# Kernel optimization log

Hardware: AMD Instinct MI355X
Metric: run time of the kernel (lower is better)

Reference implementation:

```python
import jax, jax.numpy as jnp
import numpy as np

NEG_SLOPE = 0.2  # PyG GATConv default


def _gat_conv(x, src, dst, W, a_src, a_dst, bias, concat):
    # x: [N, F_in]; W: [H*C, F_in]; a_src/a_dst: [H, C]; src/dst: [E]
    n = x.shape[0]
    H, C = a_src.shape
    h = (x @ W.T).reshape(n, H, C)                       # [N, H, C]
    al_src = (h * a_src[None]).sum(-1)                   # [N, H]
    al_dst = (h * a_dst[None]).sum(-1)                   # [N, H]
    e = jax.nn.leaky_relu(al_src[src] + al_dst[dst], NEG_SLOPE)  # [E, H]
    # scatter-softmax over incoming edges of each dst node
    m = jax.ops.segment_max(e, dst, num_segments=n)      # [N, H]
    e = jnp.exp(e - m[dst])
    denom = jax.ops.segment_sum(e, dst, num_segments=n)  # [N, H]
    alpha = e / denom[dst]                               # [E, H]
    out = jax.ops.segment_sum(alpha[:, :, None] * h[src], dst, num_segments=n)  # [N, H, C]
    if concat:
        out = out.reshape(n, H * C)
    else:
        out = out.mean(axis=1)
    return out + bias


def setup_inputs() -> dict:
    key = jax.random.key(0)
    ks = jax.random.split(key, 16)
    N, E = 20000, 640000
    IN, HID, HEADS, OUT, HLSTM, NCLS = 256, 32, 4, 64, 32, 1
    s = 0.1
    return {
        "x": jax.random.normal(ks[0], (N, IN), jnp.float32),
        "conv1_w": jax.random.normal(ks[1], (HID * HEADS, IN), jnp.float32) * s,
        "conv1_att_src": jax.random.normal(ks[2], (HEADS, HID), jnp.float32) * s,
        "conv1_att_dst": jax.random.normal(ks[3], (HEADS, HID), jnp.float32) * s,
        "conv1_bias": jnp.zeros((HID * HEADS,), jnp.float32),
        "conv2_w": jax.random.normal(ks[4], (OUT, HID * HEADS), jnp.float32) * s,
        "conv2_att_src": jax.random.normal(ks[5], (1, OUT), jnp.float32) * s,
        "conv2_att_dst": jax.random.normal(ks[6], (1, OUT), jnp.float32) * s,
        "conv2_bias": jnp.zeros((OUT,), jnp.float32),
        "lstm_w_ih": jax.random.normal(ks[7], (4 * HLSTM, OUT), jnp.float32) * s,
        "lstm_w_hh": jax.random.normal(ks[8], (4 * HLSTM, HLSTM), jnp.float32) * s,
        "lstm_b_ih": jnp.zeros((4 * HLSTM,), jnp.float32),
        "lstm_b_hh": jnp.zeros((4 * HLSTM,), jnp.float32),
        "fc_w": jax.random.normal(ks[9], (NCLS, HLSTM), jnp.float32) * s,
        "fc_b": jnp.zeros((NCLS,), jnp.float32),
        "edge_index": jax.random.randint(ks[10], (2, E), 0, N, jnp.int64),
    }


def reference(x, conv1_w, conv1_att_src, conv1_att_dst, conv1_bias,
              conv2_w, conv2_att_src, conv2_att_dst, conv2_bias,
              lstm_w_ih, lstm_w_hh, lstm_b_ih, lstm_b_hh,
              fc_w, fc_b, edge_index):
    N = x.shape[0]
    loops = jnp.arange(N, dtype=edge_index.dtype)  # add_self_loops=True (PyG default)
    src = jnp.concatenate([edge_index[0], loops])
    dst = jnp.concatenate([edge_index[1], loops])

    h = _gat_conv(x, src, dst, conv1_w, conv1_att_src, conv1_att_dst, conv1_bias, concat=True)
    h = jax.nn.elu(h)
    h = _gat_conv(h, src, dst, conv2_w, conv2_att_src, conv2_att_dst, conv2_bias, concat=False)

    # LSTM over the node sequence, batch=1 (x.view(-1, N, out_dim))
    Hs = lstm_w_hh.shape[1]
    pre = h @ lstm_w_ih.T + (lstm_b_ih + lstm_b_hh)      # [N, 4H] input projections

    def step(carry, p):
        hp, cp = carry
        g = p + hp @ lstm_w_hh.T
        i, f, gg, o = jnp.split(g, 4)
        c = jax.nn.sigmoid(f) * cp + jax.nn.sigmoid(i) * jnp.tanh(gg)
        hn = jax.nn.sigmoid(o) * jnp.tanh(c)
        return (hn, c), hn

    init = (jnp.zeros((Hs,), x.dtype), jnp.zeros((Hs,), x.dtype))
    _, seq = jax.lax.scan(step, init, pre)               # [N, H]
    out = seq @ fc_w.T + fc_b                            # [N, num_classes]
    return out[None]                                     # [1, N, num_classes]
```

## Files before the change

### kernel.cpp

```cpp
#include <hip/hip_runtime.h>
#include <hip/hip_bf16.h>
#include <hip/hip_fp16.h>
#include <cstdint>
#include <cstddef>

#define LOG2E 1.44269504088896340736f
#define SLOTW 128
#define SCAP 32

typedef float v2f __attribute__((ext_vector_type(2)));
typedef _Float16 f16x8 __attribute__((ext_vector_type(8)));
typedef float f32x4 __attribute__((ext_vector_type(4)));

__global__ __launch_bounds__(256, 2)
void gemm1_mfma(const float* __restrict__ A, const float* __restrict__ B,
                const float* __restrict__ asrc, const float* __restrict__ adst,
                float* __restrict__ als, float* __restrict__ ald,
                __half* __restrict__ Ch, int N,
                const int* __restrict__ esrc, const int* __restrict__ edst,
                int* __restrict__ cnt, unsigned short* __restrict__ slots,
                int E, int gemmBlocks) {
  if ((int)blockIdx.x >= gemmBlocks) {
    int base = ((int)blockIdx.x - gemmBlocks) * 1024 + (int)threadIdx.x * 4;
    if (base + 3 < E) {
      int4 ss = *(const int4*)(esrc + base);
      int4 dd = *(const int4*)(edst + base);
      int p0 = atomicAdd(&cnt[dd.x], 1);
      int p1 = atomicAdd(&cnt[N + dd.y], 1);
      int p2 = atomicAdd(&cnt[2 * N + dd.z], 1);
      int p3 = atomicAdd(&cnt[3 * N + dd.w], 1);
      if (p0 < SCAP) slots[(size_t)dd.x * SLOTW + p0] = (unsigned short)ss.x;
      if (p1 < SCAP) slots[(size_t)dd.y * SLOTW + 32 + p1] = (unsigned short)ss.y;
      if (p2 < SCAP) slots[(size_t)dd.z * SLOTW + 64 + p2] = (unsigned short)ss.z;
      if (p3 < SCAP) slots[(size_t)dd.w * SLOTW + 96 + p3] = (unsigned short)ss.w;
    } else if (base < E) {
      for (int t = base; t < E; ++t) {
        int s = esrc[t], d = edst[t];
        int j = t & 3;
        int pos = atomicAdd(&cnt[j * N + d], 1);
        if (pos < SCAP) slots[(size_t)d * SLOTW + j * 32 + pos] = (unsigned short)s;
      }
    }
    return;
  }
  constexpr int M = 128, K = 256, TN = 32, KB = 64;
  constexpr int LDH = 72;
  constexpr int RF = 2, CF = 2;
  constexpr int NS = K / KB;

  __shared__ __align__(16) _Float16 As[TN * LDH];
  __shared__ __align__(16) _Float16 Bs[M * LDH];

  const int tid = threadIdx.x;
  const int n0 = blockIdx.x * TN;
  const int w = tid >> 6, lane = tid & 63;
  const int lr = lane & 15, lg = lane >> 4;
  const int colbase = w * 32;

  const int ar = tid >> 3;
  const int ak = (tid & 7) * 8;
  const int gnA = n0 + ar;

  f32x4 acc[RF][CF];
#pragma unroll
  for (int rf = 0; rf < RF; ++rf)
#pragma unroll
    for (int cf = 0; cf < CF; ++cf) acc[rf][cf] = (f32x4){0.f, 0.f, 0.f, 0.f};

  float4 pa0, pa1;
  float4 pb[8];

  const float* aRow = A + (size_t)gnA * K + ak;

#define LOADG(k0)                                                              \
  do {                                                                         \
    if (gnA < N) { pa0 = *(const float4*)(aRow + (k0));                        \
                   pa1 = *(const float4*)(aRow + (k0) + 4); }                  \
    else { pa0 = make_float4(0.f,0.f,0.f,0.f); pa1 = pa0; }                    \
    _Pragma("unroll")                                                          \
    for (int c = 0; c < 4; ++c) {                                              \
      int cid = c * 256 + tid;                                                 \
      int brow = cid >> 3, bk = (cid & 7) * 8;                                 \
      const float* bp = B + (size_t)brow * K + (k0) + bk;                      \
      pb[2*c]   = *(const float4*)bp;                                          \
      pb[2*c+1] = *(const float4*)(bp + 4);                                    \
    }                                                                          \
  } while (0)

  LOADG(0);
  for (int s = 0; s < NS; ++s) {
    {
      f16x8 h;
      h[0]=(_Float16)pa0.x; h[1]=(_Float16)pa0.y; h[2]=(_Float16)pa0.z; h[3]=(_Float16)pa0.w;
      h[4]=(_Float16)pa1.x; h[5]=(_Float16)pa1.y; h[6]=(_Float16)pa1.z; h[7]=(_Float16)pa1.w;
      *(f16x8*)&As[ar * LDH + ak] = h;
#pragma unroll
      for (int c = 0; c < 4; ++c) {
        int cid = c * 256 + tid;
        int brow = cid >> 3, bk = (cid & 7) * 8;
        f16x8 hb;
        hb[0]=(_Float16)pb[2*c].x; hb[1]=(_Float16)pb[2*c].y;
        hb[2]=(_Float16)pb[2*c].z; hb[3]=(_Float16)pb[2*c].w;
        hb[4]=(_Float16)pb[2*c+1].x; hb[5]=(_Float16)pb[2*c+1].y;
        hb[6]=(_Float16)pb[2*c+1].z; hb[7]=(_Float16)pb[2*c+1].w;
        *(f16x8*)&Bs[brow * LDH + bk] = hb;
      }
    }
    __syncthreads();
    if (s + 1 < NS) LOADG((s + 1) * KB);
    {
      f16x8 af[2][RF], bf[2][CF];
#pragma unroll
      for (int ks = 0; ks < 2; ++ks) {
#pragma unroll
        for (int rf = 0; rf < RF; ++rf)
          af[ks][rf] = *(const f16x8*)&As[(rf * 16 + lr) * LDH + ks * 32 + 8 * lg];
#pragma unroll
        for (int cf = 0; cf < CF; ++cf)
          bf[ks][cf] = *(const f16x8*)&Bs[(colbase + cf * 16 + lr) * LDH + ks * 32 + 8 * lg];
      }
#pragma unroll
      for (int ks = 0; ks < 2; ++ks)
#pragma unroll
        for (int rf = 0; rf < RF; ++rf)
#pragma unroll
          for (int cf = 0; cf < CF; ++cf)
            acc[rf][cf] = __builtin_amdgcn_mfma_f32_16x16x32_f16(af[ks][rf], bf[ks][cf], acc[rf][cf], 0, 0, 0);
    }
    __syncthreads();
  }
#undef LOADG

#pragma unroll
  for (int rf = 0; rf < RF; ++rf) {
#pragma unroll
    for (int reg = 0; reg < 4; ++reg) {
      const int gr = n0 + rf * 16 + lg * 4 + reg;
      if (gr < N) {
#pragma unroll
        for (int cf = 0; cf < CF; ++cf)
          Ch[(size_t)gr * M + colbase + cf * 16 + lr] = __float2half(acc[rf][cf][reg]);
      }
    }
  }
  {
    float as_v[CF], ad_v[CF];
#pragma unroll
    for (int cf = 0; cf < CF; ++cf) {
      as_v[cf] = asrc[colbase + cf * 16 + lr];
      ad_v[cf] = adst[colbase + cf * 16 + lr];
    }
#pragma unroll
    for (int rf = 0; rf < RF; ++rf) {
#pragma unroll
      for (int reg = 0; reg < 4; ++reg) {
        const int gr = n0 + rf * 16 + lg * 4 + reg;
        float ps = acc[rf][0][reg] * as_v[0] + acc[rf][1][reg] * as_v[1];
        float pd = acc[rf][0][reg] * ad_v[0] + acc[rf][1][reg] * ad_v[1];
#pragma unroll
        for (int m = 1; m < 16; m <<= 1) { ps += __shfl_xor(ps, m); pd += __shfl_xor(pd, m); }
        if (lr == 0 && gr < N) {
          als[(size_t)gr * 4 + w] = ps;
          ald[(size_t)gr * 4 + w] = pd;
        }
      }
    }
  }
}

template<int M, int K, bool BIAS, bool AL, int H, bool HOUT, bool SCAT>
__global__ __launch_bounds__(256)
void gemm_mfma(const float* __restrict__ A, const float* __restrict__ B,
               const float* __restrict__ bias0, const float* __restrict__ bias1,
               const float* __restrict__ asrc, const float* __restrict__ adst,
               float* __restrict__ als, float* __restrict__ ald,
               float* __restrict__ C, __half* __restrict__ Ch, int N,
               const int* __restrict__ esrc, const int* __restrict__ edst,
               int* __restrict__ cnt, unsigned short* __restrict__ slots,
               int E, int gemmBlocks) {
  constexpr int TN = 64, KB = 32;
  constexpr int LDH = 40;
  constexpr int WCOL = (M >= 128) ? 2 : 1;
  constexpr int WROW = 4 / WCOL;
  constexpr int RT = TN / WROW;
  constexpr int CTW = M / WCOL;
  constexpr int RF = RT / 16;
  constexpr int CF = CTW / 16;

  __shared__ __align__(16) _Float16 As[TN * LDH];
  __shared__ __align__(16) _Float16 Bs[M * LDH];

  const int tid = threadIdx.x;
  const int n0 = blockIdx.x * TN;
  const int w = tid >> 6, lane = tid & 63;
  const int wr = w / WCOL, wc = w % WCOL;
  const int lr = lane & 15, lg = lane >> 4;

  f32x4 acc[RF][CF];
#pragma unroll
  for (int rf = 0; rf < RF; ++rf)
#pragma unroll
    for (int cf = 0; cf < CF; ++cf) acc[rf][cf] = (f32x4){0.f, 0.f, 0.f, 0.f};

  const int arow = tid >> 2, akq = (tid & 3) * 8;
  const int bcol = tid >> 1, bkq = (tid & 1) * 16;

  for (int k0 = 0; k0 < K; k0 += KB) {
    {
      int gn = n0 + arow;
      float4 v0 = make_float4(0.f, 0.f, 0.f, 0.f), v1 = v0;
      if (gn < N) {
        const float* ap = A + (size_t)gn * K + k0 + akq;
        v0 = *(const float4*)ap;
        v1 = *(const float4*)(ap + 4);
      }
      f16x8 h;
      h[0] = (_Float16)v0.x; h[1] = (_Float16)v0.y; h[2] = (_Float16)v0.z; h[3] = (_Float16)v0.w;
      h[4] = (_Float16)v1.x; h[5] = (_Float16)v1.y; h[6] = (_Float16)v1.z; h[7] = (_Float16)v1.w;
      *(f16x8*)&As[arow * LDH + akq] = h;
    }
    if (bcol < M) {
      const float* bp = B + (size_t)bcol * K + k0 + bkq;
      float4 v0 = *(const float4*)bp;
      float4 v1 = *(const float4*)(bp + 4);
      float4 v2 = *(const float4*)(bp + 8);
      float4 v3 = *(const float4*)(bp + 12);
      f16x8 h0, h1;
      h0[0] = (_Float16)v0.x; h0[1] = (_Float16)v0.y; h0[2] = (_Float16)v0.z; h0[3] = (_Float16)v0.w;
      h0[4] = (_Float16)v1.x; h0[5] = (_Float16)v1.y; h0[6] = (_Float16)v1.z; h0[7] = (_Float16)v1.w;
      h1[0] = (_Float16)v2.x; h1[1] = (_Float16)v2.y; h1[2] = (_Float16)v2.z; h1[3] = (_Float16)v2.w;
      h1[4] = (_Float16)v3.x; h1[5] = (_Float16)v3.y; h1[6] = (_Float16)v3.z; h1[7] = (_Float16)v3.w;
      *(f16x8*)&Bs[bcol * LDH + bkq] = h0;
      *(f16x8*)&Bs[bcol * LDH + bkq + 8] = h1;
    }
    __syncthreads();
    f16x8 af[RF], bf[CF];
#pragma unroll
    for (int rf = 0; rf < RF; ++rf)
      af[rf] = *(const f16x8*)&As[(wr * RT + rf * 16 + lr) * LDH + 8 * lg];
#pragma unroll
    for (int cf = 0; cf < CF; ++cf)
      bf[cf] = *(const f16x8*)&Bs[(wc * CTW + cf * 16 + lr) * LDH + 8 * lg];
#pragma unroll
    for (int rf = 0; rf < RF; ++rf)
#pragma unroll
      for (int cf = 0; cf < CF; ++cf)
        acc[rf][cf] = __builtin_amdgcn_mfma_f32_16x16x32_f16(af[rf], bf[cf], acc[rf][cf], 0, 0, 0);
    __syncthreads();
  }

  const int colbase = wc * CTW;
  float bv[CF];
#pragma unroll
  for (int cf = 0; cf < CF; ++cf) {
    if constexpr (BIAS) bv[cf] = bias0[colbase + cf * 16 + lr] + bias1[colbase + cf * 16 + lr];
    else bv[cf] = 0.f;
  }
#pragma unroll
  for (int rf = 0; rf < RF; ++rf) {
#pragma unroll
    for (int reg = 0; reg < 4; ++reg) {
      const int gr = n0 + wr * RT + rf * 16 + lg * 4 + reg;
      if (gr < N) {
#pragma unroll
        for (int cf = 0; cf < CF; ++cf) {
          float v = acc[rf][cf][reg] + bv[cf];
          if constexpr (HOUT) Ch[(size_t)gr * M + colbase + cf * 16 + lr] = __float2half(v);
          else                C[(size_t)gr * M + colbase + cf * 16 + lr] = v;
        }
      }
    }
  }
  if constexpr (AL) {
    constexpr int CPH = M / H;
    constexpr int FPH = CPH / 16;
    constexpr int HPW = CTW / CPH;
    float as_v[CF], ad_v[CF];
#pragma unroll
    for (int cf = 0; cf < CF; ++cf) {
      as_v[cf] = asrc[colbase + cf * 16 + lr];
      ad_v[cf] = adst[colbase + cf * 16 + lr];
    }
#pragma unroll
    for (int rf = 0; rf < RF; ++rf) {
#pragma unroll
      for (int reg = 0; reg < 4; ++reg) {
        const int gr = n0 + wr * RT + rf * 16 + lg * 4 + reg;
#pragma unroll
        for (int hh = 0; hh < HPW; ++hh) {
          float ps = 0.f, pd = 0.f;
#pragma unroll
          for (int f = 0; f < FPH; ++f) {
            const int cf = hh * FPH + f;
            ps = fmaf(acc[rf][cf][reg], as_v[cf], ps);
            pd = fmaf(acc[rf][cf][reg], ad_v[cf], pd);
          }
#pragma unroll
          for (int m = 1; m < 16; m <<= 1) { ps += __shfl_xor(ps, m); pd += __shfl_xor(pd, m); }
          if (lr == 0 && gr < N) {
            const int head = (colbase + hh * CPH) / CPH;
            als[(size_t)gr * H + head] = ps;
            ald[(size_t)gr * H + head] = pd;
          }
        }
      }
    }
  }
}

template<int M, int K, bool BIAS>
__global__ __launch_bounds__(256)
void gemm_nt(const float* __restrict__ A, const float* __restrict__ B,
             const float* __restrict__ bias0, const float* __restrict__ bias1,
             float* __restrict__ C, int N) {
  constexpr int TN = 64, KB = 32;
  constexpr int CT = M / 4;
  constexpr int NR = (TN * M) / 1024;
  constexpr int WT = (M * KB) / 1024;
  __shared__ __align__(16) float xs[KB][TN + 4];
  __shared__ __align__(16) float ws[KB][M + 4];
  const int tid = threadIdx.x;
  const int tc = tid % CT, tr = tid / CT;
  const int n0 = blockIdx.x * TN;
  float acc[NR][4];
#pragma unroll
  for (int r = 0; r < NR; ++r) { acc[r][0] = acc[r][1] = acc[r][2] = acc[r][3] = 0.f; }

  for (int k0 = 0; k0 < K; k0 += KB) {
#pragma unroll
    for (int u = 0; u < 2; ++u) {
      int slot = u * 256 + tid;
      int node = slot >> 3, kv = (slot & 7) * 4;
      int gn = n0 + node;
      float4 v = make_float4(0.f, 0.f, 0.f, 0.f);
      if (gn < N) v = *(const float4*)(A + (size_t)gn * K + k0 + kv);
      xs[kv + 0][node] = v.x; xs[kv + 1][node] = v.y; xs[kv + 2][node] = v.z; xs[kv + 3][node] = v.w;
    }
#pragma unroll
    for (int u = 0; u < WT; ++u) {
      int slot = u * 256 + tid;
      int col = slot >> 3, kv = (slot & 7) * 4;
      float4 v = *(const float4*)(B + (size_t)col * K + k0 + kv);
      ws[kv + 0][col] = v.x; ws[kv + 1][col] = v.y; ws[kv + 2][col] = v.z; ws[kv + 3][col] = v.w;
    }
    __syncthreads();
#pragma unroll
    for (int kk = 0; kk < KB; ++kk) {
      float4 wv = *(const float4*)&ws[kk][tc * 4];
      float4 va = *(const float4*)&xs[kk][tr * NR];
      float4 vb = va;
      if constexpr (NR == 8) vb = *(const float4*)&xs[kk][tr * NR + 4];
      float xr[NR];
      xr[0] = va.x; xr[1] = va.y; xr[2] = va.z; xr[3] = va.w;
      if constexpr (NR == 8) { xr[4] = vb.x; xr[5] = vb.y; xr[6] = vb.z; xr[7] = vb.w; }
#pragma unroll
      for (int r = 0; r < NR; ++r) {
        acc[r][0] = fmaf(xr[r], wv.x, acc[r][0]);
        acc[r][1] = fmaf(xr[r], wv.y, acc[r][1]);
        acc[r][2] = fmaf(xr[r], wv.z, acc[r][2]);
        acc[r][3] = fmaf(xr[r], wv.w, acc[r][3]);
      }
    }
    __syncthreads();
  }
  float b[4] = {0.f, 0.f, 0.f, 0.f};
  if constexpr (BIAS) {
#pragma unroll
    for (int c = 0; c < 4; ++c) b[c] = bias0[tc * 4 + c] + bias1[tc * 4 + c];
  }
#pragma unroll
  for (int r = 0; r < NR; ++r) {
    int gn = n0 + tr * NR + r;
    if (gn < N) {
      float4 o = make_float4(acc[r][0] + b[0], acc[r][1] + b[1], acc[r][2] + b[2], acc[r][3] + b[3]);
      *(float4*)(C + (size_t)gn * M + tc * 4) = o;
    }
  }
}

template<int D, int H, bool ELU, int CAP>
__global__ __launch_bounds__(D)
void conv_edge(const __half* __restrict__ hsrc, const float* __restrict__ als,
               const float* __restrict__ ald, const float* __restrict__ bias,
               const int* __restrict__ cnt, const unsigned short* __restrict__ slots,
               const int* __restrict__ esrc, const int* __restrict__ edst, int E,
               float* __restrict__ out, int N) {
  constexpr int C = D / H;
  const int n = blockIdx.x;
  const int tid = threadIdx.x;
  const int myh = tid / C;
  const int c0 = cnt[n], c1 = cnt[N + n], c2 = cnt[2 * N + n], c3 = cnt[3 * N + n];
  const int deg_r = c0 + c1 + c2 + c3;
  const int deg = deg_r + 1;
  const bool ok = (c0 <= SCAP) && (c1 <= SCAP) && (c2 <= SCAP) && (c3 <= SCAP) && (deg <= CAP);

  __shared__ __align__(16) float lw[CAP][H];
  __shared__ int sidx[CAP];
  __shared__ float red[2][H];

  float ad[H];
#pragma unroll
  for (int hh = 0; hh < H; ++hh) ad[hh] = ald[(size_t)n * H + hh];

  float acc = 0.f;
  float myinv;
  if (ok) {
    const int b0 = c0, b1 = c0 + c1, b2 = b1 + c2;
    float sm[H];
#pragma unroll
    for (int hh = 0; hh < H; ++hh) sm[hh] = 0.f;
    const unsigned short* srow = slots + (size_t)n * SLOTW;
    for (int e = tid; e < deg; e += D) {
      int s;
      if (e == 0) s = n;
      else {
        int idx = e - 1, off;
        if (idx < b0)      off = idx;
        else if (idx < b1) off = 32 + (idx - b0);
        else if (idx < b2) off = 64 + (idx - b1);
        else               off = 96 + (idx - b2);
        s = (int)srow[off];
      }
      sidx[e] = s * (D * 2);
      if constexpr (H == 4) {
        float4 a4 = *(const float4*)(als + (size_t)s * 4);
        float l0 = a4.x + ad[0]; l0 = l0 > 0.f ? l0 : 0.2f * l0;
        float l1 = a4.y + ad[1]; l1 = l1 > 0.f ? l1 : 0.2f * l1;
        float l2 = a4.z + ad[2]; l2 = l2 > 0.f ? l2 : 0.2f * l2;
        float l3 = a4.w + ad[3]; l3 = l3 > 0.f ? l3 : 0.2f * l3;
        float w0 = __builtin_amdgcn_exp2f(LOG2E * l0);
        float w1 = __builtin_amdgcn_exp2f(LOG2E * l1);
        float w2 = __builtin_amdgcn_exp2f(LOG2E * l2);
        float w3 = __builtin_amdgcn_exp2f(LOG2E * l3);
        *(float4*)&lw[e][0] = make_float4(w0, w1, w2, w3);
        sm[0] += w0; sm[1] += w1; sm[2] += w2; sm[3] += w3;
      } else {
        float x = als[s] + ad[0];
        x = x > 0.f ? x : 0.2f * x;
        float w = __builtin_amdgcn_exp2f(LOG2E * x);
        lw[e][0] = w;
        sm[0] += w;
      }
    }
#pragma unroll
    for (int hh = 0; hh < H; ++hh) {
#pragma unroll
      for (int m = 32; m >= 1; m >>= 1) sm[hh] += __shfl_xor(sm[hh], m);
    }
    if constexpr (D > 64) {
      if ((tid & 63) == 0) {
#pragma unroll
        for (int hh = 0; hh < H; ++hh) red[tid >> 6][hh] = sm[hh];
      }
      __syncthreads();
#pragma unroll
      for (int hh = 0; hh < H; ++hh) sm[hh] = red[0][hh] + red[1][hh];
    }
    myinv = 1.0f / sm[myh];
    __syncthreads();
    const char* hb = (const char*)hsrc + (size_t)tid * 2;
#pragma unroll 8
    for (int e = 0; e < deg; ++e) {
      float w = lw[e][myh];
      int ofs = sidx[e];
      float hv = __half2float(*(const __half*)(hb + ofs));
      acc = fmaf(w, hv, acc);
    }
  } else {
    float mx[H];
#pragma unroll
    for (int hh = 0; hh < H; ++hh) {
      float xs_ = als[(size_t)n * H + hh] + ad[hh];
      xs_ = xs_ > 0.f ? xs_ : 0.2f * xs_;
      mx[hh] = xs_;
    }
    for (int e = tid; e < E; e += D) {
      if (edst[e] != n) continue;
      int s = esrc[e];
#pragma unroll
      for (int hh = 0; hh < H; ++hh) {
        float x = als[(size_t)s * H + hh] + ad[hh];
        x = x > 0.f ? x : 0.2f * x;
        mx[hh] = fmaxf(mx[hh], x);
      }
    }
#pragma unroll
    for (int hh = 0; hh < H; ++hh) {
#pragma unroll
      for (int m = 32; m >= 1; m >>= 1) mx[hh] = fmaxf(mx[hh], __shfl_xor(mx[hh], m));
    }
    if constexpr (D > 64) {
      if ((tid & 63) == 0) {
#pragma unroll
        for (int hh = 0; hh < H; ++hh) red[tid >> 6][hh] = mx[hh];
      }
      __syncthreads();
#pragma unroll
      for (int hh = 0; hh < H; ++hh) mx[hh] = fmaxf(red[0][hh], red[1][hh]);
      __syncthreads();
    }
    float sm[H];
#pragma unroll
    for (int hh = 0; hh < H; ++hh) sm[hh] = 0.f;
    if (tid == 0) {
#pragma unroll
      for (int hh = 0; hh < H; ++hh) {
        float x = als[(size_t)n * H + hh] + ad[hh];
        x = x > 0.f ? x : 0.2f * x;
        sm[hh] += __builtin_amdgcn_exp2f(LOG2E * (x - mx[hh]));
      }
    }
    for (int e = tid; e < E; e += D) {
      if (edst[e] != n) continue;
      int s = esrc[e];
#pragma unroll
      for (int hh = 0; hh < H; ++hh) {
        float x = als[(size_t)s * H + hh] + ad[hh];
        x = x > 0.f ? x : 0.2f * x;
        sm[hh] += __builtin_amdgcn_exp2f(LOG2E * (x - mx[hh]));
      }
    }
#pragma unroll
    for (int hh = 0; hh < H; ++hh) {
#pragma unroll
      for (int m = 32; m >= 1; m >>= 1) sm[hh] += __shfl_xor(sm[hh], m);
    }
    if constexpr (D > 64) {
      if ((tid & 63) == 0) {
#pragma unroll
        for (int hh = 0; hh < H; ++hh) red[tid >> 6][hh] = sm[hh];
      }
      __syncthreads();
#pragma unroll
      for (int hh = 0; hh < H; ++hh) sm[hh] = red[0][hh] + red[1][hh];
    }
    const float myad = ad[myh], mym = mx[myh];
    myinv = 1.0f / sm[myh];
    {
      float x = als[(size_t)n * H + myh] + myad;
      x = x > 0.f ? x : 0.2f * x;
      float w = __builtin_amdgcn_exp2f(LOG2E * (x - mym));
      acc = fmaf(w, __half2float(hsrc[(size_t)n * D + tid]), acc);
    }
    for (int e = 0; e < E; ++e) {
      if (edst[e] != n) continue;
      int s = esrc[e];
      float x = als[(size_t)s * H + myh] + myad;
      x = x > 0.f ? x : 0.2f * x;
      float w = __builtin_amdgcn_exp2f(LOG2E * (x - mym));
      acc = fmaf(w, __half2float(hsrc[(size_t)s * D + tid]), acc);
    }
  }
  float v = fmaf(acc, myinv, bias[tid]);
  if constexpr (ELU) v = v > 0.f ? v : (__builtin_amdgcn_exp2f(LOG2E * v) - 1.0f);
  out[(size_t)n * D + tid] = v;
}

#define LSTM_S 24
#define LSTM_W 64
__global__ __attribute__((amdgpu_waves_per_eu(1, 1))) __launch_bounds__(64)
void lstm_kernel(const float* __restrict__ pre, const float* __restrict__ whh,
                 const float* __restrict__ fcw, const float* __restrict__ fcb,
                 float* __restrict__ out, int N) {
  constexpr int U = 8;
  const int lane = threadIdx.x;
  const int k = lane & 31, half = lane >> 5;
  const int row0 = k + 32 * half;
  const int row1 = 64 + k + 32 * half;

  const int t0 = blockIdx.x * LSTM_S;
  const int tb = max(0, t0 - LSTM_W);
  const int te = min(t0 + LSTM_S, N);

  v2f wp[32];
#pragma unroll
  for (int j = 0; j < 32; ++j) {
    wp[j].x = whh[row0 * 32 + j];
    wp[j].y = whh[row1 * 32 + j];
  }
  const float mult_y = half ? -LOG2E : 2.0f * LOG2E;
  const float m1 = half ? 1.0f : -2.0f;
  const float a1c = half ? 0.0f : 1.0f;
  const float myfw = fcw[k];
  const float fcb0 = fcb[0];

  float hn = 0.f, cp = 0.f;
  float c0[U], c1[U], n0[U], n1[U];
  const float* pb = pre + (size_t)tb * 128;
#pragma unroll
  for (int u = 0; u < U; ++u) {
    c0[u] = pb[(size_t)u * 128 + row0];
    c1[u] = pb[(size_t)u * 128 + row1];
  }
#pragma unroll
  for (int u = 0; u < U; ++u) {
    n0[u] = pb[(size_t)(U + u) * 128 + row0];
    n1[u] = pb[(size_t)(U + u) * 128 + row1];
  }

#pragma unroll 1
  for (int t = tb; t < te; t += U) {
#pragma unroll
    for (int u = 0; u < U; ++u) {
      v2f acc0 = {c0[u], c1[u]};
      v2f acc1 = {0.f, 0.f}, acc2 = {0.f, 0.f}, acc3 = {0.f, 0.f};
      const int hni = __float_as_int(hn);
#pragma unroll
      for (int j = 0; j < 8; ++j) {
        float s = __int_as_float(__builtin_amdgcn_readlane(hni, 32 + j));
        v2f ss = {s, s};
        acc0 = __builtin_elementwise_fma(ss, wp[j], acc0);
      }
#pragma unroll
      for (int j = 8; j < 16; ++j) {
        float s = __int_as_float(__builtin_amdgcn_readlane(hni, 32 + j));
        v2f ss = {s, s};
        acc1 = __builtin_elementwise_fma(ss, wp[j], acc1);
      }
#pragma unroll
      for (int j = 16; j < 24; ++j) {
        float s = __int_as_float(__builtin_amdgcn_readlane(hni, 32 + j));
        v2f ss = {s, s};
        acc2 = __builtin_elementwise_fma(ss, wp[j], acc2);
      }
#pragma unroll
      for (int j = 24; j < 32; ++j) {
        float s = __int_as_float(__builtin_amdgcn_readlane(hni, 32 + j));
        v2f ss = {s, s};
        acc3 = __builtin_elementwise_fma(ss, wp[j], acc3);
      }
      v2f a01 = (acc0 + acc1) + (acc2 + acc3);
      float ax = a01.x;
      float ay = a01.y;
      float e0 = __builtin_amdgcn_exp2f(-LOG2E * ax);
      float sa = __builtin_amdgcn_rcpf(1.0f + e0);
      float e1 = __builtin_amdgcn_exp2f(mult_y * ay);
      float r1 = __builtin_amdgcn_rcpf(1.0f + e1);
      float v1 = fmaf(r1, m1, a1c);
      float op2 = half ? cp : v1;
      float q = sa * op2;
      float xu = __shfl_xor(q, 32, 64);
      float c = q + xu;
      cp = c;
      float e2 = __builtin_amdgcn_exp2f(2.0f * LOG2E * c);
      float r2 = __builtin_amdgcn_rcpf(1.0f + e2);
      float tc = fmaf(r2, -2.0f, 1.0f);
      hn = v1 * tc;
      const int tt = t + u;
      if (tt >= t0) {
        float p = hn * myfw;
        p += __shfl_xor(p, 16); p += __shfl_xor(p, 8); p += __shfl_xor(p, 4);
        p += __shfl_xor(p, 2);  p += __shfl_xor(p, 1);
        if (lane == 32) out[tt] = p + fcb0;
      }
    }
#pragma unroll
    for (int u = 0; u < U; ++u) { c0[u] = n0[u]; c1[u] = n1[u]; }
    const float* nx = pre + (size_t)(t + 2 * U) * 128;
#pragma unroll
    for (int u = 0; u < U; ++u) {
      n0[u] = nx[(size_t)u * 128 + row0];
      n1[u] = nx[(size_t)u * 128 + row1];
    }
  }
}

extern "C" void kernel_launch(void* const* d_in, const int* in_sizes, int n_in,
                              void* d_out, int out_size, void* d_ws, size_t ws_size,
                              hipStream_t stream) {
  const float* x   = (const float*)d_in[0];
  const float* w1  = (const float*)d_in[1];
  const float* a1s = (const float*)d_in[2];
  const float* a1d = (const float*)d_in[3];
  const float* b1  = (const float*)d_in[4];
  const float* w2  = (const float*)d_in[5];
  const float* a2s = (const float*)d_in[6];
  const float* a2d = (const float*)d_in[7];
  const float* b2  = (const float*)d_in[8];
  const float* wih = (const float*)d_in[9];
  const float* whh = (const float*)d_in[10];
  const float* bih = (const float*)d_in[11];
  const float* bhh = (const float*)d_in[12];
  const float* fcw = (const float*)d_in[13];
  const float* fcb = (const float*)d_in[14];
  const int*   ei  = (const int*)d_in[15];
  const int N = in_sizes[0] / 256;
  const int E = in_sizes[15] / 2;
  const int* esrc = ei;
  const int* edst = ei + E;

  float* fw = (float*)d_ws;
  size_t o = 0;
  __half* h1h = (__half*)(fw + o); o += (size_t)N * 64;
  __half* h2h = (__half*)(fw + o); o += (size_t)N * 32;
  float* x2   = fw + o; o += (size_t)N * 128;
  float* h3   = fw + o; o += (size_t)N * 64;
  float* pre  = fw + o; o += (size_t)(N + 16) * 128;
  float* al1s = fw + o; o += (size_t)N * 4;
  float* al1d = fw + o; o += (size_t)N * 4;
  float* al2s = fw + o; o += (size_t)N;
  float* al2d = fw + o; o += (size_t)N;
  int* cnt = (int*)(fw + o); o += (size_t)4 * N;
  unsigned short* slots = (unsigned short*)(fw + o);

  const int eb = (E + 1023) / 1024;
  const int gb1 = (N + 31) / 32;
  const int gb = (N + 63) / 64;
  const int lstm_blocks = (N + LSTM_S - 1) / LSTM_S;

  hipMemsetAsync(cnt, 0, (size_t)4 * N * sizeof(int), stream);

  hipLaunchKernelGGL(gemm1_mfma, dim3(gb1 + eb), dim3(256), 0, stream,
                     x, w1, a1s, a1d, al1s, al1d, h1h, N,
                     esrc, edst, cnt, slots, E, gb1);

  hipLaunchKernelGGL((conv_edge<128, 4, true, 160>), dim3(N), dim3(128), 0, stream,
                     h1h, al1s, al1d, b1, cnt, slots, esrc, edst, E, x2, N);

  hipLaunchKernelGGL((gemm_mfma<64, 128, false, true, 1, true, false>),
                     dim3(gb), dim3(256), 0, stream,
                     x2, w2, (const float*)nullptr, (const float*)nullptr,
                     a2s, a2d, al2s, al2d, (float*)nullptr, h2h, N,
                     (const int*)nullptr, (const int*)nullptr, (int*)nullptr,
                     (unsigned short*)nullptr, 0, 0);
  hipLaunchKernelGGL((conv_edge<64, 1, false, 160>), dim3(N), dim3(64), 0, stream,
                     h2h, al2s, al2d, b2, cnt, slots, esrc, edst, E, h3, N);

  hipLaunchKernelGGL((gemm_nt<128, 64, true>),
                     dim3(gb), dim3(256), 0, stream,
                     h3, wih, bih, bhh, pre, N);
  hipLaunchKernelGGL(lstm_kernel, dim3(lstm_blocks), dim3(64), 0, stream,
                     pre, whh, fcw, fcb, (float*)d_out, N);
}
```

Before: 227.7 us.

## Partition edge bucketing by destination range across XCD-mapped blocks

The edge-bucketing blocks fused into the first GEMM kernel are replicated eight times. Each replica scans the same edge chunk but only processes destinations in one eighth of the node range, selected by blockIdx&7. This likely aims to keep atomics and slot writes for a given node range on one XCD/L2 under round-robin block dispatch, so they stay local. The cost is eight times the edge reads, extra blocks, and a launch_bounds occupancy hint raised from 2 to 4, which may limit GEMM registers.

```diff
diff --git a/kernel.cpp b/kernel.cpp
--- a/kernel.cpp
+++ b/kernel.cpp
@@ -12,7 +12,7 @@
 typedef _Float16 f16x8 __attribute__((ext_vector_type(8)));
 typedef float f32x4 __attribute__((ext_vector_type(4)));
 
-__global__ __launch_bounds__(256, 2)
+__global__ __launch_bounds__(256, 4)
 void gemm1_mfma(const float* __restrict__ A, const float* __restrict__ B,
                 const float* __restrict__ asrc, const float* __restrict__ adst,
                 float* __restrict__ als, float* __restrict__ ald,
@@ -21,21 +21,36 @@
                 int* __restrict__ cnt, unsigned short* __restrict__ slots,
                 int E, int gemmBlocks) {
   if ((int)blockIdx.x >= gemmBlocks) {
-    int base = ((int)blockIdx.x - gemmBlocks) * 1024 + (int)threadIdx.x * 4;
+    const int part = (int)blockIdx.x & 7;
+    const int PQ = (N + 7) >> 3;
+    const int lo = part * PQ;
+    const int hi = (lo + PQ < N) ? lo + PQ : N;
+    const int sb = (int)blockIdx.x - gemmBlocks;
+    const int chunk = sb >> 3;
+    const int base = chunk * 1024 + (int)threadIdx.x * 4;
     if (base + 3 < E) {
       int4 ss = *(const int4*)(esrc + base);
       int4 dd = *(const int4*)(edst + base);
-      int p0 = atomicAdd(&cnt[dd.x], 1);
-      int p1 = atomicAdd(&cnt[N + dd.y], 1);
-      int p2 = atomicAdd(&cnt[2 * N + dd.z], 1);
-      int p3 = atomicAdd(&cnt[3 * N + dd.w], 1);
-      if (p0 < SCAP) slots[(size_t)dd.x * SLOTW + p0] = (unsigned short)ss.x;
-      if (p1 < SCAP) slots[(size_t)dd.y * SLOTW + 32 + p1] = (unsigned short)ss.y;
-      if (p2 < SCAP) slots[(size_t)dd.z * SLOTW + 64 + p2] = (unsigned short)ss.z;
-      if (p3 < SCAP) slots[(size_t)dd.w * SLOTW + 96 + p3] = (unsigned short)ss.w;
+      if (dd.x >= lo && dd.x < hi) {
+        int p = atomicAdd(&cnt[dd.x], 1);
+        if (p < SCAP) slots[(size_t)dd.x * SLOTW + p] = (unsigned short)ss.x;
+      }
+      if (dd.y >= lo && dd.y < hi) {
+        int p = atomicAdd(&cnt[N + dd.y], 1);
+        if (p < SCAP) slots[(size_t)dd.y * SLOTW + 32 + p] = (unsigned short)ss.y;
+      }
+      if (dd.z >= lo && dd.z < hi) {
+        int p = atomicAdd(&cnt[2 * N + dd.z], 1);
+        if (p < SCAP) slots[(size_t)dd.z * SLOTW + 64 + p] = (unsigned short)ss.z;
+      }
+      if (dd.w >= lo && dd.w < hi) {
+        int p = atomicAdd(&cnt[3 * N + dd.w], 1);
+        if (p < SCAP) slots[(size_t)dd.w * SLOTW + 96 + p] = (unsigned short)ss.w;
+      }
     } else if (base < E) {
       for (int t = base; t < E; ++t) {
         int s = esrc[t], d = edst[t];
+        if (d < lo || d >= hi) continue;
         int j = t & 3;
         int pos = atomicAdd(&cnt[j * N + d], 1);
         if (pos < SCAP) slots[(size_t)d * SLOTW + j * 32 + pos] = (unsigned short)s;
@@ -710,7 +725,7 @@
 
   hipMemsetAsync(cnt, 0, (size_t)4 * N * sizeof(int), stream);
 
-  hipLaunchKernelGGL(gemm1_mfma, dim3(gb1 + eb), dim3(256), 0, stream,
+  hipLaunchKernelGGL(gemm1_mfma, dim3(gb1 + 8 * eb), dim3(256), 0, stream,
                      x, w1, a1s, a1d, al1s, al1d, h1h, N,
                      esrc, edst, cnt, slots, E, gb1);
 
```

Measured after the change: 219.6 us. 3.6% less time.
